# Performance work log

Measured on AMD Instinct MI355X. Metric: run time of the kernel, lower is better.

The kernel has to match this reference:

```python
import jax, jax.numpy as jnp
import numpy as np

WS = 8
HEADS = 12


def _dwconv(x, w, b):
    # x: (N, C, H, W); w: (C, 1, 3, 3) depthwise, zero pad 1
    y = jax.lax.conv_general_dilated(
        x, w, window_strides=(1, 1), padding=((1, 1), (1, 1)),
        dimension_numbers=("NCHW", "OIHW", "NCHW"), feature_group_count=x.shape[1])
    return y + b[None, :, None, None]


def _sepconv(x, dw, db, pw, pb):
    y = _dwconv(x, dw, db)
    # pointwise 1x1 conv: (N,C,H,W) x (O,C) -> (N,O,H,W)
    return jnp.einsum("nchw,oc->nohw", y, pw) + pb[None, :, None, None]


def _rel_pos_index(ws):
    coords = np.stack(np.meshgrid(np.arange(ws), np.arange(ws), indexing="ij"))  # (2, ws, ws)
    cf = coords.reshape(2, -1)
    rel = cf[:, :, None] - cf[:, None, :]          # (2, ws*ws, ws*ws)
    rel = rel.transpose(1, 2, 0).copy()
    rel[..., 0] += ws - 1
    rel[..., 1] += ws - 1
    rel[..., 0] *= 2 * ws - 1
    return rel.sum(-1)                             # (ws*ws, ws*ws)


def setup_inputs() -> dict:
    key = jax.random.key(0)
    ks = jax.random.split(key, 16)
    B, T, C, H, W = 2, 1, 384, 192, 192
    s = 0.02
    inp = {
        "vid": jax.random.normal(ks[0], (B, T, C, H, W), jnp.float32),
        "qd_w": jax.random.normal(ks[1], (C, 1, 3, 3), jnp.float32) * s,
        "qd_b": jnp.zeros((C,), jnp.float32),
        "qp_w": jax.random.normal(ks[2], (C, C), jnp.float32) * s,
        "qp_b": jnp.zeros((C,), jnp.float32),
        "kd_w": jax.random.normal(ks[3], (C, 1, 3, 3), jnp.float32) * s,
        "kd_b": jnp.zeros((C,), jnp.float32),
        "kp_w": jax.random.normal(ks[4], (C, C), jnp.float32) * s,
        "kp_b": jnp.zeros((C,), jnp.float32),
        "vd_w": jax.random.normal(ks[5], (C, 1, 3, 3), jnp.float32) * s,
        "vd_b": jnp.zeros((C,), jnp.float32),
        "vp_w": jax.random.normal(ks[6], (C, C), jnp.float32) * s,
        "vp_b": jnp.zeros((C,), jnp.float32),
        "rpb_table": jax.random.normal(ks[7], ((2 * WS - 1) ** 2, HEADS), jnp.float32) * s,
        "proj_w": jax.random.normal(ks[8], (C, C), jnp.float32) * s,
        "proj_b": jnp.zeros((C,), jnp.float32),
    }
    return inp


def reference(vid, qd_w, qd_b, qp_w, qp_b, kd_w, kd_b, kp_w, kp_b,
              vd_w, vd_b, vp_w, vp_b, rpb_table, proj_w, proj_b):
    B, T, C, H, W = vid.shape
    heads, ws = HEADS, WS
    hd = C // heads
    scale = hd ** -0.5
    x = vid.reshape(B * T, C, H, W)

    q = _sepconv(x, qd_w, qd_b, qp_w, qp_b) * scale
    k = _sepconv(x, kd_w, kd_b, kp_w, kp_b)
    v = _sepconv(x, vd_w, vd_b, vp_w, vp_b)

    nh, nw = H // ws, W // ws

    def win(z):  # (N, C, H, W) -> (N*nh*nw, heads, ws*ws, hd)
        N = z.shape[0]
        z = z.reshape(N, heads, hd, nh, ws, nw, ws)
        z = z.transpose(0, 3, 5, 1, 4, 6, 2)  # N, nh, nw, heads, ws, ws, hd
        return z.reshape(N * nh * nw, heads, ws * ws, hd)

    qw, kw, vw = win(q), win(k), win(v)

    # product search within window (dists = q . k), rel-pos bias softmax
    attn = jnp.einsum("nhqd,nhkd->nhqk", qw, kw)
    rp_idx = _rel_pos_index(ws)  # static (64, 64)
    bias = rpb_table[rp_idx.reshape(-1)].reshape(ws * ws, ws * ws, heads)
    bias = bias.transpose(2, 0, 1)  # (heads, 64, 64)
    attn = jax.nn.softmax(attn + bias[None], axis=-1)

    # weighted patch sum (ps=1 -> pixels)
    out = jnp.einsum("nhqk,nhkd->nhqd", attn, vw)  # (N*nh*nw, heads, ws*ws, hd)

    # un-window, merge heads into (h c) channel order, then token projection
    out = out.reshape(B * T, nh, nw, heads, ws, ws, hd)
    out = out.transpose(0, 1, 4, 2, 5, 3, 6).reshape(B * T, H, W, heads * hd)
    out = out @ proj_w.T + proj_b

    # fold (ps=1, stride0=1): identity overlap-add, zvid == 1
    out = out.transpose(0, 3, 1, 2).reshape(B, T, C, H, W)
    return out
```

## Files before the change

### kernel.cpp

```cpp
#include <hip/hip_runtime.h>

#define CCH 384
#define HH 192
#define WWD 192
#define NIMG 2
#define HWP (HH * WWD)
#define PTOT (NIMG * HWP)
#define HEADS 12
#define HD 32
#define NWIN 24
#define WINS 576
#define EELEM ((size_t)NIMG * CCH * HWP)
#define WMAT 147456

typedef __attribute__((ext_vector_type(8))) short bh8;
typedef __attribute__((ext_vector_type(8))) unsigned short us8;
typedef __attribute__((ext_vector_type(4))) unsigned short us4;
typedef __attribute__((ext_vector_type(4))) float fx4;

__device__ __forceinline__ unsigned short f2bf(float f) {
    unsigned u = __float_as_uint(f);
    u += 0x7fffu + ((u >> 16) & 1u);
    return (unsigned short)(u >> 16);
}

__device__ __forceinline__ void gload16(const void* g, void* l) {
    __builtin_amdgcn_global_load_lds(
        (const __attribute__((address_space(1))) void*)g,
        (__attribute__((address_space(3))) void*)l, 16, 0, 0);
}

__global__ __launch_bounds__(256) void wcvt(
    const float* __restrict__ a, const float* __restrict__ b,
    const float* __restrict__ c, const float* __restrict__ d,
    unsigned short* __restrict__ o)
{
    int idx8 = (blockIdx.x * 256 + threadIdx.x) * 8;
    int which = idx8 / WMAT;
    int loc = idx8 - which * WMAT;
    const float* s = (which == 0) ? a : (which == 1) ? b : (which == 2) ? c : d;
    float4 v0 = *(const float4*)(s + loc);
    float4 v1 = *(const float4*)(s + loc + 4);
    us8 ov;
    ov[0] = f2bf(v0.x); ov[1] = f2bf(v0.y); ov[2] = f2bf(v0.z); ov[3] = f2bf(v0.w);
    ov[4] = f2bf(v1.x); ov[5] = f2bf(v1.y); ov[6] = f2bf(v1.z); ov[7] = f2bf(v1.w);
    *(us8*)(o + idx8) = ov;
}

__global__ __launch_bounds__(256) void wprep(
    const float* __restrict__ q, const float* __restrict__ k,
    const float* __restrict__ v, float* __restrict__ o)
{
    int idx = blockIdx.x * 256 + threadIdx.x;
    if (idx >= 3 * 9 * CCH) return;
    int ten = idx / (9 * CCH);
    int rem = idx - ten * (9 * CCH);
    int tap = rem / CCH;
    int c   = rem - tap * CCH;
    const float* s = (ten == 0) ? q : (ten == 1) ? k : v;
    o[idx] = s[c * 9 + tap];
}

__global__ __launch_bounds__(256) void dwgather(
    const float* __restrict__ x,
    const float* __restrict__ wt,
    const float* __restrict__ qb, const float* __restrict__ kb,
    const float* __restrict__ vb,
    unsigned short* __restrict__ oq, unsigned short* __restrict__ ok,
    unsigned short* __restrict__ ov)
{
    __shared__ float halo[64 * 121];

    int bid = blockIdx.x;
    int b = (bid & 7) * 864 + (bid >> 3);
    int wtx  = b % 24;
    int strip = b / 24;
    int chv  = strip % 6;
    int nwy  = strip / 6;
    int wy   = nwy % 24;
    int n    = nwy / 24;

    int h0 = wy * 8, w0 = wtx * 8;
    int tid = threadIdx.x;
    int c   = tid & 63;
    int pxg = tid >> 6;
    int cg  = chv * 64 + c;
    int widx = n * WINS + wy * NWIN + wtx;

    const float* xbase = x + (size_t)n * CCH * HWP + (size_t)(chv * 64) * HWP;

    for (int j = tid; j < 1920; j += 256) {
        int seg = j % 3;
        int t   = j / 3;
        int rr  = t % 10;
        int cc  = t / 10;
        int hr  = h0 - 1 + rr;
        int cb  = w0 - 2 + seg * 4;
        float4 val = make_float4(0.f, 0.f, 0.f, 0.f);
        if (hr >= 0 && hr < HH) {
            const float* p = xbase + (size_t)cc * HWP + (size_t)hr * WWD;
            if (cb >= 0 && cb + 4 <= WWD) {
                val = *(const float4*)(p + cb);
            } else {
                if (cb + 0 >= 0 && cb + 0 < WWD) val.x = p[cb + 0];
                if (cb + 1 >= 0 && cb + 1 < WWD) val.y = p[cb + 1];
                if (cb + 2 >= 0 && cb + 2 < WWD) val.z = p[cb + 2];
                if (cb + 3 >= 0 && cb + 3 < WWD) val.w = p[cb + 3];
            }
        }
        int hb = cc * 121 + rr * 12 + seg * 4;
        halo[hb + 0] = val.x;
        halo[hb + 1] = val.y;
        halo[hb + 2] = val.z;
        halo[hb + 3] = val.w;
    }

    float wq[9], wk[9], wv[9];
#pragma unroll
    for (int t = 0; t < 9; ++t) {
        wq[t] = wt[t * CCH + cg];
        wk[t] = wt[9 * CCH + t * CCH + cg];
        wv[t] = wt[18 * CCH + t * CCH + cg];
    }
    float bqv = qb[cg], bkv = kb[cg], bvv = vb[cg];

    __syncthreads();

    const int hbase = c * 121 + (2 * pxg) * 12;
    float r0[10], r1[10], r2[10];
#pragma unroll
    for (int cc = 0; cc < 10; ++cc) r0[cc] = halo[hbase + cc + 1];
#pragma unroll
    for (int cc = 0; cc < 10; ++cc) r1[cc] = halo[hbase + 12 + cc + 1];
#pragma unroll
    for (int cc = 0; cc < 10; ++cc) r2[cc] = halo[hbase + 24 + cc + 1];

    size_t ob0 = ((size_t)widx * 64 + pxg * 16) * CCH + cg;

#pragma unroll
    for (int pc = 0; pc < 8; ++pc) {
        float sq = 0.f, sk = 0.f, sv = 0.f;
#pragma unroll
        for (int dc = 0; dc < 3; ++dc) {
            float x0 = r0[pc + dc], x1 = r1[pc + dc], x2 = r2[pc + dc];
            sq = fmaf(x0, wq[dc], sq);     sk = fmaf(x0, wk[dc], sk);     sv = fmaf(x0, wv[dc], sv);
            sq = fmaf(x1, wq[3 + dc], sq); sk = fmaf(x1, wk[3 + dc], sk); sv = fmaf(x1, wv[3 + dc], sv);
            sq = fmaf(x2, wq[6 + dc], sq); sk = fmaf(x2, wk[6 + dc], sk); sv = fmaf(x2, wv[6 + dc], sv);
        }
        size_t o = ob0 + (size_t)pc * CCH;
        oq[o] = f2bf(sq + bqv);
        ok[o] = f2bf(sk + bkv);
        ov[o] = f2bf(sv + bvv);
    }

#pragma unroll
    for (int cc = 0; cc < 10; ++cc) r0[cc] = halo[hbase + 36 + cc + 1];

#pragma unroll
    for (int pc = 0; pc < 8; ++pc) {
        float sq = 0.f, sk = 0.f, sv = 0.f;
#pragma unroll
        for (int dc = 0; dc < 3; ++dc) {
            float x0 = r1[pc + dc], x1 = r2[pc + dc], x2 = r0[pc + dc];
            sq = fmaf(x0, wq[dc], sq);     sk = fmaf(x0, wk[dc], sk);     sv = fmaf(x0, wv[dc], sv);
            sq = fmaf(x1, wq[3 + dc], sq); sk = fmaf(x1, wk[3 + dc], sk); sv = fmaf(x1, wv[3 + dc], sv);
            sq = fmaf(x2, wq[6 + dc], sq); sk = fmaf(x2, wk[6 + dc], sk); sv = fmaf(x2, wv[6 + dc], sv);
        }
        size_t o = ob0 + (size_t)(8 + pc) * CCH;
        oq[o] = f2bf(sq + bqv);
        ok[o] = f2bf(sk + bkv);
        ov[o] = f2bf(sv + bvv);
    }
}

template<int ORIENT>
__global__ __launch_bounds__(256) void pw_gemm(
    const unsigned short* __restrict__ Y, const unsigned short* __restrict__ Wb,
    const float* __restrict__ bias, float scale,
    unsigned short* __restrict__ outb, float* __restrict__ outf)
{
    __shared__ unsigned short Wt[2][128][32];
    __shared__ unsigned short Yt[2][128][32];

    int tid = threadIdx.x;
    int pp0 = blockIdx.x * 128;
    int cm0 = blockIdx.y * 128;
    int lid = tid & 63, wid = tid >> 6;
    int wr = wid >> 1, wc = wid & 1;
    int li = lid & 15, g = lid >> 4;

    int srow = (lid >> 2);
    int scol = (lid & 3) * 8;

    fx4 acc[4][4];
#pragma unroll
    for (int i = 0; i < 4; ++i)
#pragma unroll
        for (int j = 0; j < 4; ++j) acc[i][j] = (fx4){0.f, 0.f, 0.f, 0.f};

    typedef unsigned short (*tile3)[128][32];
    tile3 A3 = (ORIENT == 1) ? Wt : Yt;
    tile3 B3 = (ORIENT == 1) ? Yt : Wt;

    const unsigned short* Wg0 = Wb + (size_t)(cm0 + wid * 32 + srow) * CCH + scol;
    const unsigned short* Yg0 = Y  + (size_t)(pp0 + wid * 32 + srow) * CCH + scol;

#pragma unroll
    for (int qi = 0; qi < 2; ++qi) {
        gload16(Wg0 + (size_t)qi * 16 * CCH, &Wt[0][wid * 32 + qi * 16][0]);
        gload16(Yg0 + (size_t)qi * 16 * CCH, &Yt[0][wid * 32 + qi * 16][0]);
    }
    __syncthreads();

    for (int kt = 0; kt < 12; ++kt) {
        int cur = kt & 1;
        if (kt < 11) {
            int k1 = (kt + 1) * 32;
#pragma unroll
            for (int qi = 0; qi < 2; ++qi) {
                gload16(Wg0 + (size_t)qi * 16 * CCH + k1, &Wt[cur ^ 1][wid * 32 + qi * 16][0]);
                gload16(Yg0 + (size_t)qi * 16 * CCH + k1, &Yt[cur ^ 1][wid * 32 + qi * 16][0]);
            }
        }

        bh8 a[4], b[4];
#pragma unroll
        for (int mf = 0; mf < 4; ++mf)
            a[mf] = *(const bh8*)&A3[cur][wr * 64 + mf * 16 + li][g * 8];
#pragma unroll
        for (int nf = 0; nf < 4; ++nf)
            b[nf] = *(const bh8*)&B3[cur][wc * 64 + nf * 16 + li][g * 8];
#pragma unroll
        for (int mf = 0; mf < 4; ++mf)
#pragma unroll
            for (int nf = 0; nf < 4; ++nf)
                acc[mf][nf] = __builtin_amdgcn_mfma_f32_16x16x32_bf16(
                    a[mf], b[nf], acc[mf][nf], 0, 0, 0);

        __syncthreads();
    }

    if (ORIENT == 1) {
#pragma unroll
        for (int mf = 0; mf < 4; ++mf) {
            int c = cm0 + wr * 64 + mf * 16 + g * 4;
            float4 bv = *(const float4*)&bias[c];
#pragma unroll
            for (int nf = 0; nf < 4; ++nf) {
                int p = pp0 + wc * 64 + nf * 16 + li;
                us4 o;
                o[0] = f2bf((acc[mf][nf][0] + bv.x) * scale);
                o[1] = f2bf((acc[mf][nf][1] + bv.y) * scale);
                o[2] = f2bf((acc[mf][nf][2] + bv.z) * scale);
                o[3] = f2bf((acc[mf][nf][3] + bv.w) * scale);
                *(us4*)(outb + (size_t)p * CCH + c) = o;
            }
        }
    } else if (ORIENT == 2) {
#pragma unroll
        for (int nf = 0; nf < 4; ++nf) {
            int c = cm0 + wc * 64 + nf * 16 + li;
            float bv = bias[c];
#pragma unroll
            for (int mf = 0; mf < 4; ++mf) {
                int p = pp0 + wr * 64 + mf * 16 + g * 4;
                int n = p / HWP;
                int pl = p - n * HWP;
                us4 o;
                o[0] = f2bf(acc[mf][nf][0] + bv);
                o[1] = f2bf(acc[mf][nf][1] + bv);
                o[2] = f2bf(acc[mf][nf][2] + bv);
                o[3] = f2bf(acc[mf][nf][3] + bv);
                *(us4*)(outb + (size_t)(n * CCH + c) * HWP + pl) = o;
            }
        }
    } else {
#pragma unroll
        for (int nf = 0; nf < 4; ++nf) {
            int c = cm0 + wc * 64 + nf * 16 + li;
            float bv = bias[c];
#pragma unroll
            for (int mf = 0; mf < 4; ++mf) {
                int p = pp0 + wr * 64 + mf * 16 + g * 4;
                int n = p / HWP;
                int rem = p - n * HWP;
                int win = rem >> 6, t = rem & 63;
                int h = (win / NWIN) * 8 + (t >> 3);
                int w = (win % NWIN) * 8 + (t & 7);
                float4 o;
                o.x = acc[mf][nf][0] + bv;
                o.y = acc[mf][nf][1] + bv;
                o.z = acc[mf][nf][2] + bv;
                o.w = acc[mf][nf][3] + bv;
                *(float4*)(outf + (size_t)(n * CCH + c) * HWP + h * WWD + w) = o;
            }
        }
    }
}

__global__ __launch_bounds__(256) void attn(
    const unsigned short* __restrict__ q, const unsigned short* __restrict__ k,
    const unsigned short* __restrict__ v, const float* __restrict__ rpb,
    unsigned short* __restrict__ o)
{
    __shared__ float rpbs[225 * HEADS];
    __shared__ unsigned short Pl[4][64][72];

    int tid = threadIdx.x, lid = tid & 63, wid = tid >> 6;
    int wl = blockIdx.x;
    int n = wl / WINS, winl = wl - n * WINS;
    int li = lid & 15, g = lid >> 4;

    for (int i = tid; i < 225 * HEADS; i += 256) rpbs[i] = rpb[i];
    __syncthreads();

    const fx4 z = (fx4){0.f, 0.f, 0.f, 0.f};

    for (int hq = wid; hq < HEADS; hq += 4) {
        const unsigned short* qp = q + (size_t)(wl * 64) * CCH + hq * HD + g * 8;
        const unsigned short* kp = k + (size_t)(wl * 64) * CCH + hq * HD + g * 8;
        bh8 aq[4], bk[4];
#pragma unroll
        for (int mf = 0; mf < 4; ++mf)
            aq[mf] = *(const bh8*)(qp + (size_t)(mf * 16 + li) * CCH);
#pragma unroll
        for (int nf = 0; nf < 4; ++nf)
            bk[nf] = *(const bh8*)(kp + (size_t)(nf * 16 + li) * CCH);

        fx4 s[4][4];
#pragma unroll
        for (int mf = 0; mf < 4; ++mf)
#pragma unroll
            for (int nf = 0; nf < 4; ++nf)
                s[mf][nf] = __builtin_amdgcn_mfma_f32_16x16x32_bf16(aq[mf], bk[nf], z, 0, 0, 0);

#pragma unroll
        for (int mf = 0; mf < 4; ++mf)
#pragma unroll
            for (int nf = 0; nf < 4; ++nf)
#pragma unroll
                for (int r = 0; r < 4; ++r) {
                    int tq = mf * 16 + g * 4 + r, tk = nf * 16 + li;
                    int dy = (tq >> 3) - (tk >> 3) + 7;
                    int dx = (tq & 7) - (tk & 7) + 7;
                    s[mf][nf][r] += rpbs[(dy * 15 + dx) * HEADS + hq];
                }

        float inv_[4][4];
#pragma unroll
        for (int mf = 0; mf < 4; ++mf)
#pragma unroll
            for (int r = 0; r < 4; ++r) {
                float m = s[mf][0][r];
#pragma unroll
                for (int nf = 1; nf < 4; ++nf) m = fmaxf(m, s[mf][nf][r]);
                m = fmaxf(m, __shfl_xor(m, 1));
                m = fmaxf(m, __shfl_xor(m, 2));
                m = fmaxf(m, __shfl_xor(m, 4));
                m = fmaxf(m, __shfl_xor(m, 8));
                float sum = 0.f;
#pragma unroll
                for (int nf = 0; nf < 4; ++nf) {
                    float e = __expf(s[mf][nf][r] - m);
                    s[mf][nf][r] = e;
                    sum += e;
                }
                sum += __shfl_xor(sum, 1);
                sum += __shfl_xor(sum, 2);
                sum += __shfl_xor(sum, 4);
                sum += __shfl_xor(sum, 8);
                inv_[mf][r] = 1.f / sum;
            }

#pragma unroll
        for (int mf = 0; mf < 4; ++mf)
#pragma unroll
            for (int nf = 0; nf < 4; ++nf)
#pragma unroll
                for (int r = 0; r < 4; ++r)
                    Pl[wid][mf * 16 + g * 4 + r][nf * 16 + li] =
                        f2bf(s[mf][nf][r] * inv_[mf][r]);

        fx4 o2[2][4];
#pragma unroll
        for (int m2 = 0; m2 < 2; ++m2)
#pragma unroll
            for (int nf = 0; nf < 4; ++nf) o2[m2][nf] = z;
#pragma unroll
        for (int ks = 0; ks < 2; ++ks) {
            bh8 av[2], bp[4];
#pragma unroll
            for (int m2 = 0; m2 < 2; ++m2)
                av[m2] = *(const bh8*)(v + (size_t)(n * CCH + hq * HD + m2 * 16 + li) * HWP
                                         + winl * 64 + ks * 32 + g * 8);
#pragma unroll
            for (int nf = 0; nf < 4; ++nf)
                bp[nf] = *(const bh8*)&Pl[wid][nf * 16 + li][ks * 32 + g * 8];
#pragma unroll
            for (int m2 = 0; m2 < 2; ++m2)
#pragma unroll
                for (int nf = 0; nf < 4; ++nf)
                    o2[m2][nf] = __builtin_amdgcn_mfma_f32_16x16x32_bf16(
                        av[m2], bp[nf], o2[m2][nf], 0, 0, 0);
        }
#pragma unroll
        for (int nf = 0; nf < 4; ++nf) {
            int tq = nf * 16 + li;
#pragma unroll
            for (int m2 = 0; m2 < 2; ++m2) {
                int d = hq * HD + m2 * 16 + g * 4;
                us4 ov;
                ov[0] = f2bf(o2[m2][nf][0]);
                ov[1] = f2bf(o2[m2][nf][1]);
                ov[2] = f2bf(o2[m2][nf][2]);
                ov[3] = f2bf(o2[m2][nf][3]);
                *(us4*)(o + (size_t)(wl * 64 + tq) * CCH + d) = ov;
            }
        }
    }
}

extern "C" void kernel_launch(void* const* d_in, const int* in_sizes, int n_in,
                              void* d_out, int out_size, void* d_ws, size_t ws_size,
                              hipStream_t stream) {
    const float* vid  = (const float*)d_in[0];
    const float* qd_w = (const float*)d_in[1];
    const float* qd_b = (const float*)d_in[2];
    const float* qp_w = (const float*)d_in[3];
    const float* qp_b = (const float*)d_in[4];
    const float* kd_w = (const float*)d_in[5];
    const float* kd_b = (const float*)d_in[6];
    const float* kp_w = (const float*)d_in[7];
    const float* kp_b = (const float*)d_in[8];
    const float* vd_w = (const float*)d_in[9];
    const float* vd_b = (const float*)d_in[10];
    const float* vp_w = (const float*)d_in[11];
    const float* vp_b = (const float*)d_in[12];
    const float* rpb  = (const float*)d_in[13];
    const float* pj_w = (const float*)d_in[14];
    const float* pj_b = (const float*)d_in[15];

    unsigned short* ws16 = (unsigned short*)d_ws;
    unsigned short* tr0 = ws16 + 3 * EELEM;
    unsigned short* tr1 = ws16 + 4 * EELEM;
    unsigned short* tr2 = ws16 + 5 * EELEM;
    unsigned short* Wb  = ws16 + 6 * EELEM;
    float* dwT          = (float*)(Wb + 4 * WMAT);
    unsigned short* qb  = ws16;
    unsigned short* kb  = ws16 + EELEM;
    unsigned short* vb  = ws16 + 2 * EELEM;
    unsigned short* ob  = tr0;

    wcvt<<<288, 256, 0, stream>>>(qp_w, kp_w, vp_w, pj_w, Wb);
    wprep<<<41, 256, 0, stream>>>(qd_w, kd_w, vd_w, dwT);
    dwgather<<<NIMG * WINS * 6, 256, 0, stream>>>(
        vid, dwT, qd_b, kd_b, vd_b, tr0, tr1, tr2);

    dim3 gg(PTOT / 128, 3);
    const float scale = 0.17677669529663687f;
    pw_gemm<1><<<gg, 256, 0, stream>>>(tr0, Wb,             qp_b, scale, qb, nullptr);
    pw_gemm<1><<<gg, 256, 0, stream>>>(tr1, Wb + WMAT,      kp_b, 1.0f,  kb, nullptr);
    pw_gemm<2><<<gg, 256, 0, stream>>>(tr2, Wb + 2 * WMAT,  vp_b, 1.0f,  vb, nullptr);

    attn<<<NIMG * WINS, 256, 0, stream>>>(qb, kb, vb, rpb, ob);

    pw_gemm<3><<<gg, 256, 0, stream>>>(ob, Wb + 3 * WMAT, pj_b, 1.0f, nullptr, (float*)d_out);
}
```

Before: 412.4 us.

## Load depthwise halo rows directly to registers and precompute expanded attention bias

The depthwise kernel no longer stages a halo tile in shared memory behind a barrier. Each thread now loads its own four input rows straight from global memory into registers with float4 reads, which removes LDS traffic and the sync but reads overlapping halo rows from global or cache several times. A new small kernel expands the relative-position bias table into a dense per-head 64x64 matrix, so the attention kernel no longer copies the table into shared memory or computes gather indices. Instead it reads one vector of four bias values per fragment from global memory.

Measured after the change: 448.5 us. 1.09x slower.

```diff
diff --git a/kernel.cpp b/kernel.cpp
--- a/kernel.cpp
+++ b/kernel.cpp
@@ -61,6 +61,18 @@
     o[idx] = s[c * 9 + tap];
 }
 
+__global__ __launch_bounds__(256) void biasx(
+    const float* __restrict__ rpb, float* __restrict__ Bx)
+{
+    int idx = blockIdx.x * 256 + threadIdx.x;
+    int h  = idx >> 12;
+    int tk = (idx >> 6) & 63;
+    int tq = idx & 63;
+    int dy = (tq >> 3) - (tk >> 3) + 7;
+    int dx = (tq & 7) - (tk & 7) + 7;
+    Bx[idx] = rpb[(dy * 15 + dx) * HEADS + h];
+}
+
 __global__ __launch_bounds__(256) void dwgather(
     const float* __restrict__ x,
     const float* __restrict__ wt,
@@ -69,8 +81,6 @@
     unsigned short* __restrict__ oq, unsigned short* __restrict__ ok,
     unsigned short* __restrict__ ov)
 {
-    __shared__ float halo[64 * 121];
-
     int bid = blockIdx.x;
     int b = (bid & 7) * 864 + (bid >> 3);
     int wtx  = b % 24;
@@ -82,38 +92,10 @@
 
     int h0 = wy * 8, w0 = wtx * 8;
     int tid = threadIdx.x;
-    int c   = tid & 63;
-    int pxg = tid >> 6;
+    int c    = tid & 63;
+    int rgrp = tid >> 6;
     int cg  = chv * 64 + c;
     int widx = n * WINS + wy * NWIN + wtx;
-
-    const float* xbase = x + (size_t)n * CCH * HWP + (size_t)(chv * 64) * HWP;
-
-    for (int j = tid; j < 1920; j += 256) {
-        int seg = j % 3;
-        int t   = j / 3;
-        int rr  = t % 10;
-        int cc  = t / 10;
-        int hr  = h0 - 1 + rr;
-        int cb  = w0 - 2 + seg * 4;
-        float4 val = make_float4(0.f, 0.f, 0.f, 0.f);
-        if (hr >= 0 && hr < HH) {
-            const float* p = xbase + (size_t)cc * HWP + (size_t)hr * WWD;
-            if (cb >= 0 && cb + 4 <= WWD) {
-                val = *(const float4*)(p + cb);
-            } else {
-                if (cb + 0 >= 0 && cb + 0 < WWD) val.x = p[cb + 0];
-                if (cb + 1 >= 0 && cb + 1 < WWD) val.y = p[cb + 1];
-                if (cb + 2 >= 0 && cb + 2 < WWD) val.z = p[cb + 2];
-                if (cb + 3 >= 0 && cb + 3 < WWD) val.w = p[cb + 3];
-            }
-        }
-        int hb = cc * 121 + rr * 12 + seg * 4;
-        halo[hb + 0] = val.x;
-        halo[hb + 1] = val.y;
-        halo[hb + 2] = val.z;
-        halo[hb + 3] = val.w;
-    }
 
     float wq[9], wk[9], wv[9];
 #pragma unroll
@@ -124,25 +106,37 @@
     }
     float bqv = qb[cg], bkv = kb[cg], bvv = vb[cg];
 
-    __syncthreads();
-
-    const int hbase = c * 121 + (2 * pxg) * 12;
-    float r0[10], r1[10], r2[10];
-#pragma unroll
-    for (int cc = 0; cc < 10; ++cc) r0[cc] = halo[hbase + cc + 1];
-#pragma unroll
-    for (int cc = 0; cc < 10; ++cc) r1[cc] = halo[hbase + 12 + cc + 1];
-#pragma unroll
-    for (int cc = 0; cc < 10; ++cc) r2[cc] = halo[hbase + 24 + cc + 1];
-
-    size_t ob0 = ((size_t)widx * 64 + pxg * 16) * CCH + cg;
+    const float* xrow = x + (size_t)n * CCH * HWP + (size_t)cg * HWP + (w0 - 4);
+    bool okl = (wtx > 0), okr = (wtx < NWIN - 1);
+
+    auto ldrow = [&](float* dst, int hr) {
+        const float* p = xrow + (size_t)hr * WWD;
+        bool okh = (hr >= 0) && (hr < HH);
+        float4 v0 = (okh && okl) ? *(const float4*)(p)      : make_float4(0, 0, 0, 0);
+        float4 v1 = okh          ? *(const float4*)(p + 4)  : make_float4(0, 0, 0, 0);
+        float4 v2 = okh          ? *(const float4*)(p + 8)  : make_float4(0, 0, 0, 0);
+        float4 v3 = (okh && okr) ? *(const float4*)(p + 12) : make_float4(0, 0, 0, 0);
+        dst[0] = v0.x; dst[1] = v0.y; dst[2]  = v0.z; dst[3]  = v0.w;
+        dst[4] = v1.x; dst[5] = v1.y; dst[6]  = v1.z; dst[7]  = v1.w;
+        dst[8] = v2.x; dst[9] = v2.y; dst[10] = v2.z; dst[11] = v2.w;
+        dst[12] = v3.x; dst[13] = v3.y; dst[14] = v3.z; dst[15] = v3.w;
+    };
+
+    int r0 = 2 * rgrp;
+    float ra[16], rb[16], rc[16], rd[16];
+    ldrow(ra, h0 + r0 - 1);
+    ldrow(rb, h0 + r0);
+    ldrow(rc, h0 + r0 + 1);
+    ldrow(rd, h0 + r0 + 2);
+
+    size_t ob0 = ((size_t)widx * 64 + r0 * 8) * CCH + cg;
 
 #pragma unroll
     for (int pc = 0; pc < 8; ++pc) {
         float sq = 0.f, sk = 0.f, sv = 0.f;
 #pragma unroll
         for (int dc = 0; dc < 3; ++dc) {
-            float x0 = r0[pc + dc], x1 = r1[pc + dc], x2 = r2[pc + dc];
+            float x0 = ra[pc + dc + 3], x1 = rb[pc + dc + 3], x2 = rc[pc + dc + 3];
             sq = fmaf(x0, wq[dc], sq);     sk = fmaf(x0, wk[dc], sk);     sv = fmaf(x0, wv[dc], sv);
             sq = fmaf(x1, wq[3 + dc], sq); sk = fmaf(x1, wk[3 + dc], sk); sv = fmaf(x1, wv[3 + dc], sv);
             sq = fmaf(x2, wq[6 + dc], sq); sk = fmaf(x2, wk[6 + dc], sk); sv = fmaf(x2, wv[6 + dc], sv);
@@ -154,14 +148,11 @@
     }
 
 #pragma unroll
-    for (int cc = 0; cc < 10; ++cc) r0[cc] = halo[hbase + 36 + cc + 1];
-
-#pragma unroll
     for (int pc = 0; pc < 8; ++pc) {
         float sq = 0.f, sk = 0.f, sv = 0.f;
 #pragma unroll
         for (int dc = 0; dc < 3; ++dc) {
-            float x0 = r1[pc + dc], x1 = r2[pc + dc], x2 = r0[pc + dc];
+            float x0 = rb[pc + dc + 3], x1 = rc[pc + dc + 3], x2 = rd[pc + dc + 3];
             sq = fmaf(x0, wq[dc], sq);     sk = fmaf(x0, wk[dc], sk);     sv = fmaf(x0, wv[dc], sv);
             sq = fmaf(x1, wq[3 + dc], sq); sk = fmaf(x1, wk[3 + dc], sk); sv = fmaf(x1, wv[3 + dc], sv);
             sq = fmaf(x2, wq[6 + dc], sq); sk = fmaf(x2, wk[6 + dc], sk); sv = fmaf(x2, wv[6 + dc], sv);
@@ -300,10 +291,9 @@
 
 __global__ __launch_bounds__(256) void attn(
     const unsigned short* __restrict__ q, const unsigned short* __restrict__ k,
-    const unsigned short* __restrict__ v, const float* __restrict__ rpb,
+    const unsigned short* __restrict__ v, const float* __restrict__ Bx,
     unsigned short* __restrict__ o)
 {
-    __shared__ float rpbs[225 * HEADS];
     __shared__ unsigned short Pl[4][64][72];
 
     int tid = threadIdx.x, lid = tid & 63, wid = tid >> 6;
@@ -311,9 +301,6 @@
     int n = wl / WINS, winl = wl - n * WINS;
     int li = lid & 15, g = lid >> 4;
 
-    for (int i = tid; i < 225 * HEADS; i += 256) rpbs[i] = rpb[i];
-    __syncthreads();
-
     const fx4 z = (fx4){0.f, 0.f, 0.f, 0.f};
 
     for (int hq = wid; hq < HEADS; hq += 4) {
@@ -337,14 +324,11 @@
 #pragma unroll
         for (int mf = 0; mf < 4; ++mf)
 #pragma unroll
-            for (int nf = 0; nf < 4; ++nf)
-#pragma unroll
-                for (int r = 0; r < 4; ++r) {
-                    int tq = mf * 16 + g * 4 + r, tk = nf * 16 + li;
-                    int dy = (tq >> 3) - (tk >> 3) + 7;
-                    int dx = (tq & 7) - (tk & 7) + 7;
-                    s[mf][nf][r] += rpbs[(dy * 15 + dx) * HEADS + hq];
-                }
+            for (int nf = 0; nf < 4; ++nf) {
+                fx4 bv = *(const fx4*)&Bx[((size_t)hq * 64 + nf * 16 + li) * 64
+                                          + mf * 16 + g * 4];
+                s[mf][nf] += bv;
+            }
 
         float inv_[4][4];
 #pragma unroll
@@ -446,6 +430,7 @@
     unsigned short* tr2 = ws16 + 5 * EELEM;
     unsigned short* Wb  = ws16 + 6 * EELEM;
     float* dwT          = (float*)(Wb + 4 * WMAT);
+    float* Bx           = dwT + 3 * 9 * CCH;
     unsigned short* qb  = ws16;
     unsigned short* kb  = ws16 + EELEM;
     unsigned short* vb  = ws16 + 2 * EELEM;
@@ -453,6 +438,7 @@
 
     wcvt<<<288, 256, 0, stream>>>(qp_w, kp_w, vp_w, pj_w, Wb);
     wprep<<<41, 256, 0, stream>>>(qd_w, kd_w, vd_w, dwT);
+    biasx<<<192, 256, 0, stream>>>(rpb, Bx);
     dwgather<<<NIMG * WINS * 6, 256, 0, stream>>>(
         vid, dwT, qd_b, kd_b, vd_b, tr0, tr1, tr2);
 
@@ -462,7 +448,7 @@
     pw_gemm<1><<<gg, 256, 0, stream>>>(tr1, Wb + WMAT,      kp_b, 1.0f,  kb, nullptr);
     pw_gemm<2><<<gg, 256, 0, stream>>>(tr2, Wb + 2 * WMAT,  vp_b, 1.0f,  vb, nullptr);
 
-    attn<<<NIMG * WINS, 256, 0, stream>>>(qb, kb, vb, rpb, ob);
+    attn<<<NIMG * WINS, 256, 0, stream>>>(qb, kb, vb, Bx, ob);
 
     pw_gemm<3><<<gg, 256, 0, stream>>>(ob, Wb + 3 * WMAT, pj_b, 1.0f, nullptr, (float*)d_out);
 }
```

## Stage GEMM epilogues through LDS and precompute expanded rel-pos bias

Applied to the files above, without the earlier changes.

The pointwise GEMM epilogues for orientations 1 and 2 now write bf16 tiles into a padded LDS buffer that aliases the operand tiles, then store 16-byte coalesced rows to global memory instead of scattered 8-byte stores. The relative-position bias is expanded once per call into a dense (heads,64,64) float table inside a merged prep kernel, so the attention kernel loads it as float4 vectors instead of staging the 225x12 table into LDS per block and doing index arithmetic. The weight-convert, depthwise-transpose and bias-expansion launches are merged into one kernel. The cost is an extra barrier in the GEMM epilogue and about 196 KB of bias reads from global or cache per attention block.

Result: no change. 405.4 us (-1.7%).

```diff
diff --git a/kernel.cpp b/kernel.cpp
--- a/kernel.cpp
+++ b/kernel.cpp
@@ -30,35 +30,45 @@
         (__attribute__((address_space(3))) void*)l, 16, 0, 0);
 }
 
-__global__ __launch_bounds__(256) void wcvt(
-    const float* __restrict__ a, const float* __restrict__ b,
-    const float* __restrict__ c, const float* __restrict__ d,
-    unsigned short* __restrict__ o)
+__global__ __launch_bounds__(256) void prep(
+    const float* __restrict__ qp, const float* __restrict__ kp,
+    const float* __restrict__ vp, const float* __restrict__ pj,
+    const float* __restrict__ qd, const float* __restrict__ kd,
+    const float* __restrict__ vd, const float* __restrict__ rpb,
+    unsigned short* __restrict__ Wb, float* __restrict__ dwT,
+    float* __restrict__ Bx)
 {
-    int idx8 = (blockIdx.x * 256 + threadIdx.x) * 8;
-    int which = idx8 / WMAT;
-    int loc = idx8 - which * WMAT;
-    const float* s = (which == 0) ? a : (which == 1) ? b : (which == 2) ? c : d;
-    float4 v0 = *(const float4*)(s + loc);
-    float4 v1 = *(const float4*)(s + loc + 4);
-    us8 ov;
-    ov[0] = f2bf(v0.x); ov[1] = f2bf(v0.y); ov[2] = f2bf(v0.z); ov[3] = f2bf(v0.w);
-    ov[4] = f2bf(v1.x); ov[5] = f2bf(v1.y); ov[6] = f2bf(v1.z); ov[7] = f2bf(v1.w);
-    *(us8*)(o + idx8) = ov;
-}
-
-__global__ __launch_bounds__(256) void wprep(
-    const float* __restrict__ q, const float* __restrict__ k,
-    const float* __restrict__ v, float* __restrict__ o)
-{
-    int idx = blockIdx.x * 256 + threadIdx.x;
-    if (idx >= 3 * 9 * CCH) return;
-    int ten = idx / (9 * CCH);
-    int rem = idx - ten * (9 * CCH);
-    int tap = rem / CCH;
-    int c   = rem - tap * CCH;
-    const float* s = (ten == 0) ? q : (ten == 1) ? k : v;
-    o[idx] = s[c * 9 + tap];
+    int bx = blockIdx.x;
+    if (bx < 288) {
+        int idx8 = (bx * 256 + threadIdx.x) * 8;
+        int which = idx8 / WMAT;
+        int loc = idx8 - which * WMAT;
+        const float* s = (which == 0) ? qp : (which == 1) ? kp : (which == 2) ? vp : pj;
+        float4 v0 = *(const float4*)(s + loc);
+        float4 v1 = *(const float4*)(s + loc + 4);
+        us8 ov;
+        ov[0] = f2bf(v0.x); ov[1] = f2bf(v0.y); ov[2] = f2bf(v0.z); ov[3] = f2bf(v0.w);
+        ov[4] = f2bf(v1.x); ov[5] = f2bf(v1.y); ov[6] = f2bf(v1.z); ov[7] = f2bf(v1.w);
+        *(us8*)(Wb + idx8) = ov;
+    } else if (bx < 329) {
+        int idx = (bx - 288) * 256 + threadIdx.x;
+        if (idx < 3 * 9 * CCH) {
+            int ten = idx / (9 * CCH);
+            int rem = idx - ten * (9 * CCH);
+            int tap = rem / CCH;
+            int c   = rem - tap * CCH;
+            const float* s = (ten == 0) ? qd : (ten == 1) ? kd : vd;
+            dwT[idx] = s[c * 9 + tap];
+        }
+    } else {
+        int idx = (bx - 329) * 256 + threadIdx.x;
+        int h  = idx >> 12;
+        int tk = (idx >> 6) & 63;
+        int tq = idx & 63;
+        int dy = (tq >> 3) - (tk >> 3) + 7;
+        int dx = (tq & 7) - (tk & 7) + 7;
+        Bx[idx] = rpb[(dy * 15 + dx) * HEADS + h];
+    }
 }
 
 __global__ __launch_bounds__(256) void dwgather(
@@ -179,8 +189,12 @@
     const float* __restrict__ bias, float scale,
     unsigned short* __restrict__ outb, float* __restrict__ outf)
 {
-    __shared__ unsigned short Wt[2][128][32];
-    __shared__ unsigned short Yt[2][128][32];
+    __shared__ __align__(16) char smem[33792];
+    typedef unsigned short (*tile3)[128][32];
+    tile3 Wt = (tile3)smem;
+    tile3 Yt = (tile3)(smem + 16384);
+    typedef unsigned short (*tep_t)[132];
+    tep_t T16 = (tep_t)smem;
 
     int tid = threadIdx.x;
     int pp0 = blockIdx.x * 128;
@@ -198,7 +212,6 @@
 #pragma unroll
         for (int j = 0; j < 4; ++j) acc[i][j] = (fx4){0.f, 0.f, 0.f, 0.f};
 
-    typedef unsigned short (*tile3)[128][32];
     tile3 A3 = (ORIENT == 1) ? Wt : Yt;
     tile3 B3 = (ORIENT == 1) ? Yt : Wt;
 
@@ -243,36 +256,52 @@
     if (ORIENT == 1) {
 #pragma unroll
         for (int mf = 0; mf < 4; ++mf) {
-            int c = cm0 + wr * 64 + mf * 16 + g * 4;
-            float4 bv = *(const float4*)&bias[c];
+            int cl = wr * 64 + mf * 16 + g * 4;
+            float4 bv = *(const float4*)&bias[cm0 + cl];
 #pragma unroll
             for (int nf = 0; nf < 4; ++nf) {
-                int p = pp0 + wc * 64 + nf * 16 + li;
+                int pl = wc * 64 + nf * 16 + li;
                 us4 o;
                 o[0] = f2bf((acc[mf][nf][0] + bv.x) * scale);
                 o[1] = f2bf((acc[mf][nf][1] + bv.y) * scale);
                 o[2] = f2bf((acc[mf][nf][2] + bv.z) * scale);
                 o[3] = f2bf((acc[mf][nf][3] + bv.w) * scale);
-                *(us4*)(outb + (size_t)p * CCH + c) = o;
-            }
+                *(us4*)&T16[pl][cl] = o;
+            }
+        }
+        __syncthreads();
+#pragma unroll
+        for (int it = 0; it < 8; ++it) {
+            int row = it * 16 + wid * 4 + (lid >> 4);
+            int col = (lid & 15) * 8;
+            us8 vv = *(const us8*)&T16[row][col];
+            *(us8*)(outb + (size_t)(pp0 + row) * CCH + cm0 + col) = vv;
         }
     } else if (ORIENT == 2) {
 #pragma unroll
         for (int nf = 0; nf < 4; ++nf) {
-            int c = cm0 + wc * 64 + nf * 16 + li;
-            float bv = bias[c];
+            int cl = wc * 64 + nf * 16 + li;
+            float bv = bias[cm0 + cl];
 #pragma unroll
             for (int mf = 0; mf < 4; ++mf) {
-                int p = pp0 + wr * 64 + mf * 16 + g * 4;
-                int n = p / HWP;
-                int pl = p - n * HWP;
+                int pl = wr * 64 + mf * 16 + g * 4;
                 us4 o;
                 o[0] = f2bf(acc[mf][nf][0] + bv);
                 o[1] = f2bf(acc[mf][nf][1] + bv);
                 o[2] = f2bf(acc[mf][nf][2] + bv);
                 o[3] = f2bf(acc[mf][nf][3] + bv);
-                *(us4*)(outb + (size_t)(n * CCH + c) * HWP + pl) = o;
-            }
+                *(us4*)&T16[cl][pl] = o;
+            }
+        }
+        __syncthreads();
+        int n = pp0 / HWP;
+        int pl0 = pp0 - n * HWP;
+#pragma unroll
+        for (int it = 0; it < 8; ++it) {
+            int row = it * 16 + wid * 4 + (lid >> 4);
+            int col = (lid & 15) * 8;
+            us8 vv = *(const us8*)&T16[row][col];
+            *(us8*)(outb + (size_t)(n * CCH + cm0 + row) * HWP + pl0 + col) = vv;
         }
     } else {
 #pragma unroll
@@ -300,10 +329,9 @@
 
 __global__ __launch_bounds__(256) void attn(
     const unsigned short* __restrict__ q, const unsigned short* __restrict__ k,
-    const unsigned short* __restrict__ v, const float* __restrict__ rpb,
+    const unsigned short* __restrict__ v, const float* __restrict__ Bx,
     unsigned short* __restrict__ o)
 {
-    __shared__ float rpbs[225 * HEADS];
     __shared__ unsigned short Pl[4][64][72];
 
     int tid = threadIdx.x, lid = tid & 63, wid = tid >> 6;
@@ -311,9 +339,6 @@
     int n = wl / WINS, winl = wl - n * WINS;
     int li = lid & 15, g = lid >> 4;
 
-    for (int i = tid; i < 225 * HEADS; i += 256) rpbs[i] = rpb[i];
-    __syncthreads();
-
     const fx4 z = (fx4){0.f, 0.f, 0.f, 0.f};
 
     for (int hq = wid; hq < HEADS; hq += 4) {
@@ -337,14 +362,11 @@
 #pragma unroll
         for (int mf = 0; mf < 4; ++mf)
 #pragma unroll
-            for (int nf = 0; nf < 4; ++nf)
-#pragma unroll
-                for (int r = 0; r < 4; ++r) {
-                    int tq = mf * 16 + g * 4 + r, tk = nf * 16 + li;
-                    int dy = (tq >> 3) - (tk >> 3) + 7;
-                    int dx = (tq & 7) - (tk & 7) + 7;
-                    s[mf][nf][r] += rpbs[(dy * 15 + dx) * HEADS + hq];
-                }
+            for (int nf = 0; nf < 4; ++nf) {
+                fx4 bv = *(const fx4*)&Bx[((size_t)hq * 64 + nf * 16 + li) * 64
+                                          + mf * 16 + g * 4];
+                s[mf][nf] += bv;
+            }
 
         float inv_[4][4];
 #pragma unroll
@@ -446,13 +468,14 @@
     unsigned short* tr2 = ws16 + 5 * EELEM;
     unsigned short* Wb  = ws16 + 6 * EELEM;
     float* dwT          = (float*)(Wb + 4 * WMAT);
+    float* Bx           = dwT + 3 * 9 * CCH;
     unsigned short* qb  = ws16;
     unsigned short* kb  = ws16 + EELEM;
     unsigned short* vb  = ws16 + 2 * EELEM;
     unsigned short* ob  = tr0;
 
-    wcvt<<<288, 256, 0, stream>>>(qp_w, kp_w, vp_w, pj_w, Wb);
-    wprep<<<41, 256, 0, stream>>>(qd_w, kd_w, vd_w, dwT);
+    prep<<<521, 256, 0, stream>>>(qp_w, kp_w, vp_w, pj_w,
+                                  qd_w, kd_w, vd_w, rpb, Wb, dwT, Bx);
     dwgather<<<NIMG * WINS * 6, 256, 0, stream>>>(
         vid, dwT, qd_b, kd_b, vd_b, tr0, tr1, tr2);
 
@@ -462,7 +485,7 @@
     pw_gemm<1><<<gg, 256, 0, stream>>>(tr1, Wb + WMAT,      kp_b, 1.0f,  kb, nullptr);
     pw_gemm<2><<<gg, 256, 0, stream>>>(tr2, Wb + 2 * WMAT,  vp_b, 1.0f,  vb, nullptr);
 
-    attn<<<NIMG * WINS, 256, 0, stream>>>(qb, kb, vb, rpb, ob);
+    attn<<<NIMG * WINS, 256, 0, stream>>>(qb, kb, vb, Bx, ob);
 
     pw_gemm<3><<<gg, 256, 0, stream>>>(ob, Wb + 3 * WMAT, pj_b, 1.0f, nullptr, (float*)d_out);
 }
```
